# Kernel tuning notes

Hardware: AMD Instinct MI355X
Metric: run time of the kernel (lower is better)

Reference implementation:

```python
import jax, jax.numpy as jnp
import numpy as np

K = 4096
N = 11008
GROUP_SIZE = 128
NUM_GROUPS = K // GROUP_SIZE
BATCH = 4
SEQ = 2048


def setup_inputs() -> dict:
    key = jax.random.key(0)
    kx, kw, ks = jax.random.split(key, 3)
    x = jax.random.normal(kx, (BATCH, SEQ, K), dtype=jnp.float16)
    # packed uint8 bytes, each holding two INT4 values (stored as int32)
    weight_packed = jax.random.randint(kw, (N, K // 2), 0, 256, dtype=jnp.int32)
    # positive group-wise scales ~ abs(randn)*0.1 -> uniform*0.1 is fine statistically
    scales = (jax.random.uniform(ks, (N, NUM_GROUPS), dtype=jnp.float32) * 0.1).astype(jnp.float16)
    return {"x": x, "weight_packed": weight_packed, "scales": scales}


def _dequantize(weight_packed, scales):
    # unpack: low nibble first, then high nibble -> (N, K) values in [0, 15]
    low = weight_packed & 15
    high = (weight_packed >> 4) & 15
    w_int = jnp.stack([low, high], axis=-1).reshape(weight_packed.shape[0], -1)  # (N, K)
    # symmetric dequant with implicit zero-point 8, group-wise scales
    scales_expanded = jnp.repeat(scales, GROUP_SIZE, axis=1)  # (N, K)
    return scales_expanded * (w_int.astype(jnp.float16) - jnp.float16(8.0))


def reference(x, weight_packed, scales):
    # Y = X @ W_dequant.T : (B, S, K) x (N, K) -> (B, S, N)
    w_dequant = _dequantize(weight_packed, scales)  # (N, K) fp16
    out = jnp.einsum('bsk,nk->bsn', x, w_dequant)
    return out.astype(jnp.float16)
```

## Files before the change

### kernel.cpp

```cpp
#include <hip/hip_runtime.h>
#include <stdint.h>


namespace {

typedef unsigned int u32;
typedef unsigned short u16;
typedef __attribute__((ext_vector_type(8))) short bf16x8;
typedef __attribute__((ext_vector_type(4))) float f32x4;
typedef __attribute__((ext_vector_type(4))) u32 u32x4;

constexpr int Mt = 8192;
constexpr int Nt = 11008;
constexpr int Kt = 4096;
constexpr int KP = Kt / 2;
constexpr int NG = 32;
constexpr int BM = 256;
constexpr int BN = 256;
constexpr int BK = 64;
constexpr int THREADS = 512;
constexpr int GRID = (Mt / BM) * (Nt / BN);
constexpr int NKT = Kt / BK;
constexpr int NB_CNT = Nt / BN;

__device__ __forceinline__ u16 f2bf(float f) {
  u32 u = __float_as_uint(f);
  return (u16)((u + 0x7FFFu + ((u >> 16) & 1u)) >> 16);
}
__device__ __forceinline__ u32 pk2bf(float a, float b) {
  return (u32)f2bf(a) | ((u32)f2bf(b) << 16);
}
__device__ __forceinline__ u32 dqpair(u32 b, float s, float c) {
  float f0 = (float)(b & 15u);
  float f1 = (float)((b >> 4) & 15u);
  return pk2bf(fmaf(f0, s, c), fmaf(f1, s, c));
}
__device__ __forceinline__ void async16(const void* g, void* l) {
  __builtin_amdgcn_global_load_lds(
      (const __attribute__((address_space(1))) u32*)g,
      (__attribute__((address_space(3))) u32*)l, 16, 0, 0);
}

__global__ __launch_bounds__(256) void cvt_x(const float* __restrict__ X,
                                             u32* __restrict__ O) {
  const int total = Mt * Kt / 4;
  for (int j = blockIdx.x * 256 + threadIdx.x; j < total;
       j += (int)(gridDim.x * 256)) {
    float4 v = ((const float4*)X)[j];
    ((uint2*)O)[j] = make_uint2(pk2bf(v.x, v.y), pk2bf(v.z, v.w));
  }
}

__global__ __launch_bounds__(256) void cvt_w(const int* __restrict__ W,
                                             const float* __restrict__ S,
                                             u32* __restrict__ O) {
  const int total = Nt * KP / 4;
  for (int j = blockIdx.x * 256 + threadIdx.x; j < total;
       j += (int)(gridDim.x * 256)) {
    int4 v = ((const int4*)W)[j];
    int vv[4] = {v.x, v.y, v.z, v.w};
    const int j0 = j * 4;
    const int row = j0 >> 11;
    const int jj = j0 & 2047;
    const float* sr = S + (size_t)row * NG;
    u32x4 o;
    #pragma unroll
    for (int e = 0; e < 4; ++e) {
      float s = sr[(jj + e) >> 6];
      o[e] = dqpair((u32)vv[e], s, -8.f * s);
    }
    ((u32x4*)O)[j] = o;
  }
}

__global__ __launch_bounds__(THREADS, 2) void gemm8p(
    const u16* __restrict__ Xb, const u16* __restrict__ Wb,
    float* __restrict__ Y) {
  __shared__ __align__(16) unsigned char smem[131072];

  const int tid  = (int)threadIdx.x;
  const int lane = tid & 63;
  const int wid  = tid >> 6;
  const int wm   = wid >> 2;
  const int wn   = wid & 3;

  const int bid = (int)blockIdx.x;
  const int wg  = (bid & 7) * (GRID / 8) + (bid >> 3);
  const int band = wg / 344;
  const int r    = wg - band * 344;
  int mb, nb;
  if (r < 320) {
    const int qn = r >> 5;
    const int w  = r & 31;
    mb = band * 8 + (w >> 2);
    nb = qn * 4 + (w & 3);
  } else {
    const int r2 = r - 320;
    const int q3 = r2 / 3;
    mb = band * 8 + q3;
    nb = 40 + (r2 - q3 * 3);
  }
  const int m0  = mb * BM;
  const int n0  = nb * BN;

  const int srow = tid >> 3;
  const int sswz = (tid & 7) ^ (srow & 7);
  const u16* aRow = Xb + (size_t)(m0 + srow) * Kt + sswz * 8;
  const u16* bRow = Wb + (size_t)(n0 + (srow >> 5) * 64 + (srow & 31)) * Kt + sswz * 8;
  const int ldst = tid * 16;

  const int frow = lane & 15;
  const int fk   = lane >> 4;
  const int s0o  = ((fk ^ (lane & 7)) << 4);
  const int s1o  = (((4 + fk) ^ (lane & 7)) << 4);
  const int aRdC = (wm * 64 + frow) * 128;
  const int bRdC = (wn * 32 + frow) * 128;

  f32x4 acc[8][4];
  #pragma unroll
  for (int i = 0; i < 8; ++i)
    #pragma unroll
    for (int j = 0; j < 4; ++j) acc[i][j] = f32x4{0.f, 0.f, 0.f, 0.f};

  #define GATE(n) asm volatile("s_waitcnt vmcnt(" #n ")" ::: "memory")
  #define BARR()  asm volatile("s_barrier" ::: "memory")

  #define STAGE_A(g, buf, kt)                                                  \
    do {                                                                       \
      unsigned char* d_ = smem + (buf) * 32768 + (g) * 16384 + ldst;           \
      const u16* s_ = aRow + (size_t)((g) * 64) * Kt + (kt) * 64;              \
      async16(s_, d_);                                                         \
      async16(s_ + (size_t)128 * Kt, d_ + 8192);                               \
    } while (0)
  #define STAGE_B(p, buf, kt)                                                  \
    do {                                                                       \
      unsigned char* d_ = smem + 65536 + (buf) * 32768 + (p) * 16384 + ldst;   \
      const u16* s_ = bRow + (size_t)((p) * 32) * Kt + (kt) * 64;              \
      async16(s_, d_);                                                         \
      async16(s_ + (size_t)128 * Kt, d_ + 8192);                               \
    } while (0)

  #define LD_A(dst, g, buf)                                                    \
    do {                                                                       \
      const unsigned char* b_ = smem + (buf) * 32768 + (g) * 16384 + aRdC;     \
      _Pragma("unroll")                                                        \
      for (int q_ = 0; q_ < 4; ++q_) {                                         \
        dst[q_][0] = *(const bf16x8*)(b_ + q_ * 2048 + s0o);                   \
        dst[q_][1] = *(const bf16x8*)(b_ + q_ * 2048 + s1o);                   \
      }                                                                        \
    } while (0)
  #define LD_B(dst, p, buf)                                                    \
    do {                                                                       \
      const unsigned char* b_ =                                                \
          smem + 65536 + (buf) * 32768 + (p) * 16384 + bRdC;                   \
      _Pragma("unroll")                                                        \
      for (int q_ = 0; q_ < 2; ++q_) {                                         \
        dst[q_][0] = *(const bf16x8*)(b_ + q_ * 2048 + s0o);                   \
        dst[q_][1] = *(const bf16x8*)(b_ + q_ * 2048 + s1o);                   \
      }                                                                        \
    } while (0)

  #define MM_G(FG, FNP, A_, B_, GN)                                            \
    do {                                                                       \
      BARR();                                                                  \
      __builtin_amdgcn_s_setprio(1);                                           \
      _Pragma("unroll")                                                        \
      for (int kk_ = 0; kk_ < 2; ++kk_)                                        \
        _Pragma("unroll")                                                      \
        for (int fm_ = 0; fm_ < 4; ++fm_)                                      \
          _Pragma("unroll")                                                    \
          for (int fn_ = 0; fn_ < 2; ++fn_)                                    \
            acc[(FG) * 4 + fm_][(FNP) * 2 + fn_] =                             \
                __builtin_amdgcn_mfma_f32_16x16x32_bf16(                       \
                    A_[fm_][kk_], B_[fn_][kk_],                                \
                    acc[(FG) * 4 + fm_][(FNP) * 2 + fn_], 0, 0, 0);            \
      __builtin_amdgcn_s_setprio(0);                                           \
      if ((GN) == 6) { asm volatile("s_waitcnt vmcnt(6)" ::: "memory"); }      \
      else if ((GN) == 0) { asm volatile("s_waitcnt vmcnt(0)" ::: "memory"); } \
      BARR();                                                                  \
    } while (0)

  #define TILE(BUF, T, GN_LAST)                                                \
    do {                                                                       \
      LD_A(af, 0, BUF);                                                        \
      LD_B(b0, 0, BUF);                                                        \
      STAGE_A(1, BUF ^ 1, (T) + 1);                                            \
      MM_G(0, 0, af, b0, -1);                                                  \
      LD_B(b1, 1, BUF);                                                        \
      STAGE_A(0, BUF, (T) + 2);                                                \
      MM_G(0, 1, af, b1, -1);                                                  \
      LD_A(af, 1, BUF);                                                        \
      STAGE_B(0, BUF, (T) + 2);                                                \
      MM_G(1, 0, af, b0, -1);                                                  \
      STAGE_B(1, BUF, (T) + 2);                                                \
      MM_G(1, 1, af, b1, GN_LAST);                                             \
    } while (0)

  bf16x8 af[4][2], b0[2][2], b1[2][2];

  STAGE_A(0, 0, 0);
  STAGE_B(0, 0, 0);
  STAGE_B(1, 0, 0);
  STAGE_A(1, 0, 0);
  STAGE_A(0, 1, 1);
  STAGE_B(0, 1, 1);
  STAGE_B(1, 1, 1);
  GATE(6);
  BARR();

  #pragma unroll 1
  for (int t0 = 0; t0 < NKT - 2; t0 += 2) {
    TILE(0, t0, 6);
    TILE(1, t0 + 1, 6);
  }

  {
    LD_A(af, 0, 0);
    LD_B(b0, 0, 0);
    STAGE_A(1, 1, 63);
    MM_G(0, 0, af, b0, -1);
    LD_B(b1, 1, 0);
    MM_G(0, 1, af, b1, -1);
    LD_A(af, 1, 0);
    MM_G(1, 0, af, b0, -1);
    MM_G(1, 1, af, b1, 0);
  }
  {
    LD_A(af, 0, 1);
    LD_B(b0, 0, 1);
    MM_G(0, 0, af, b0, -1);
    LD_B(b1, 1, 1);
    MM_G(0, 1, af, b1, -1);
    LD_A(af, 1, 1);
    MM_G(1, 0, af, b0, -1);
    MM_G(1, 1, af, b1, -1);
  }

  #undef GATE
  #undef BARR
  #undef STAGE_A
  #undef STAGE_B
  #undef LD_A
  #undef LD_B
  #undef MM_G
  #undef TILE

  #pragma unroll
  for (int fm = 0; fm < 8; ++fm) {
    #pragma unroll
    for (int r2 = 0; r2 < 4; ++r2) {
      const size_t mrow = (size_t)(m0 + wm * 128 + fm * 16 + fk * 4 + r2) * Nt;
      #pragma unroll
      for (int fn = 0; fn < 4; ++fn) {
        Y[mrow + (size_t)(n0 + wn * 64 + fn * 16 + frow)] = acc[fm][fn][r2];
      }
    }
  }
}

__global__ __launch_bounds__(512) void gemm_fused(
    const float* __restrict__ Xf, const int* __restrict__ W,
    const float* __restrict__ S, float* __restrict__ Y) {
  constexpr int FBN = 128;
  constexpr int FNB = Nt / FBN;
  constexpr int FBK = 64;
  constexpr int FNKT = Kt / FBK;
  __shared__ __align__(16) unsigned char Alds[BM * FBK * 2];
  __shared__ __align__(16) unsigned char Blds[FBN * FBK * 2];

  const int tid = (int)threadIdx.x;
  const int lane = tid & 63;
  const int wid = tid >> 6;
  const int wm = wid >> 1;
  const int wn = wid & 1;

  const int bid = (int)blockIdx.x;
  const int fgrid = (Mt / BM) * FNB;
  const int wg = (bid & 7) * (fgrid / 8) + (bid >> 3);
  const int mb = wg / FNB;
  const int nb = wg - mb * FNB;
  const int m0 = mb * BM;
  const int n0 = nb * FBN;

  const int frow = lane & 15;
  const int fk = lane >> 4;
  const int fswz = (lane & 7) << 4;
  const unsigned char* aRd = Alds + (wm * 64 + frow) * 128;
  const unsigned char* bRd = Blds + (wn * 64 + frow) * 128;

  f32x4 acc[4][4];
  #pragma unroll
  for (int i = 0; i < 4; ++i)
    #pragma unroll
    for (int j = 0; j < 4; ++j) acc[i][j] = f32x4{0.f, 0.f, 0.f, 0.f};

  const int arow = tid >> 3, acol = tid & 7;
  const float* fA = Xf + (size_t)(m0 + arow) * Kt + acol * 8;
  unsigned char* fAD = Alds + arow * 128 + ((acol ^ (arow & 7)) << 4);
  const int nloc = tid >> 3, c4 = tid & 7;
  const int* fB0 = W + (size_t)(n0 + nloc) * KP + c4 * 4;
  const int* fB1 = fB0 + (size_t)64 * KP;
  const float* sp0 = S + (size_t)(n0 + nloc) * NG;
  const float* sp1 = sp0 + (size_t)64 * NG;
  unsigned char* fBD0 = Blds + nloc * 128 + ((c4 ^ (nloc & 7)) << 4);
  unsigned char* fBD1 = fBD0 + 64 * 128;

  #pragma unroll 1
  for (int kt = 0; kt < FNKT; ++kt) {
    const int k0 = kt * FBK;
    #pragma unroll
    for (int p = 0; p < 4; ++p) {
      float4 x0 = *(const float4*)(fA + (size_t)p * 64 * Kt + k0);
      float4 x1 = *(const float4*)(fA + (size_t)p * 64 * Kt + k0 + 4);
      u32x4 q;
      q[0] = pk2bf(x0.x, x0.y); q[1] = pk2bf(x0.z, x0.w);
      q[2] = pk2bf(x1.x, x1.y); q[3] = pk2bf(x1.z, x1.w);
      *(u32x4*)(fAD + p * 64 * 128) = q;
    }
    const int g = k0 >> 7;
    const float s0 = sp0[g], s1 = sp1[g];
    const float c0 = -8.f * s0, c1 = -8.f * s1;
    const int4 w0 = *(const int4*)(fB0 + (k0 >> 1));
    const int4 w1 = *(const int4*)(fB1 + (k0 >> 1));
    u32x4 q0, q1;
    q0[0] = dqpair((u32)w0.x, s0, c0); q0[1] = dqpair((u32)w0.y, s0, c0);
    q0[2] = dqpair((u32)w0.z, s0, c0); q0[3] = dqpair((u32)w0.w, s0, c0);
    q1[0] = dqpair((u32)w1.x, s1, c1); q1[1] = dqpair((u32)w1.y, s1, c1);
    q1[2] = dqpair((u32)w1.z, s1, c1); q1[3] = dqpair((u32)w1.w, s1, c1);
    *(u32x4*)fBD0 = q0;
    *(u32x4*)fBD1 = q1;

    __syncthreads();

    #pragma unroll
    for (int kk = 0; kk < 2; ++kk) {
      const int koff = (kk * 64 + fk * 16) ^ fswz;
      bf16x8 af[4], bfr[4];
      #pragma unroll
      for (int fm = 0; fm < 4; ++fm)
        af[fm] = *(const bf16x8*)(aRd + fm * 16 * 128 + koff);
      #pragma unroll
      for (int fn = 0; fn < 4; ++fn)
        bfr[fn] = *(const bf16x8*)(bRd + fn * 16 * 128 + koff);
      #pragma unroll
      for (int fm = 0; fm < 4; ++fm)
        #pragma unroll
        for (int fn = 0; fn < 4; ++fn)
          acc[fm][fn] = __builtin_amdgcn_mfma_f32_16x16x32_bf16(
              af[fm], bfr[fn], acc[fm][fn], 0, 0, 0);
    }
    __syncthreads();
  }

  #pragma unroll
  for (int fm = 0; fm < 4; ++fm) {
    #pragma unroll
    for (int r = 0; r < 4; ++r) {
      const size_t mrow = (size_t)(m0 + wm * 64 + fm * 16 + fk * 4 + r) * Nt;
      #pragma unroll
      for (int fn = 0; fn < 4; ++fn)
        Y[mrow + (size_t)(n0 + wn * 64 + fn * 16 + frow)] = acc[fm][fn][r];
    }
  }
}

}

extern "C" void kernel_launch(void* const* d_in, const int* in_sizes, int n_in,
                              void* d_out, int out_size, void* d_ws, size_t ws_size,
                              hipStream_t stream) {
  (void)in_sizes; (void)n_in; (void)out_size;
  const float* X = (const float*)d_in[0];
  const int* W   = (const int*)d_in[1];
  const float* S = (const float*)d_in[2];
  float* Y       = (float*)d_out;

  const size_t xbytes = (size_t)Mt * Kt * 2;
  const size_t wbytes = (size_t)Nt * Kt * 2;

  if (ws_size >= xbytes + wbytes) {
    u16* Xb = (u16*)d_ws;
    u16* Wb = (u16*)((char*)d_ws + xbytes);
    cvt_x<<<dim3(2048), dim3(256), 0, stream>>>(X, (u32*)Xb);
    cvt_w<<<dim3(2048), dim3(256), 0, stream>>>(W, S, (u32*)Wb);
    gemm8p<<<dim3(GRID), dim3(THREADS), 0, stream>>>(Xb, Wb, Y);
  } else {
    gemm_fused<<<dim3((Mt / BM) * (Nt / 128)), dim3(512), 0, stream>>>(X, W, S, Y);
  }
}
```

Measured before the change: 676.4 us.

## Double-buffer register fragments to prefetch next tile's LDS reads across phases

```diff
diff --git a/kernel.cpp b/kernel.cpp
--- a/kernel.cpp
+++ b/kernel.cpp
@@ -73,7 +73,7 @@
   }
 }
 
-__global__ __launch_bounds__(THREADS, 2) void gemm8p(
+__global__ __launch_bounds__(THREADS, 2) void gemmrl(
     const u16* __restrict__ Xb, const u16* __restrict__ Wb,
     float* __restrict__ Y) {
   __shared__ __align__(16) unsigned char smem[131072];
@@ -160,9 +160,8 @@
       }                                                                        \
     } while (0)
 
-  #define MM_G(FG, FNP, A_, B_, GN)                                            \
-    do {                                                                       \
-      BARR();                                                                  \
+  #define MMQ(FG, FNP, A_, B_)                                                 \
+    do {                                                                       \
       __builtin_amdgcn_s_setprio(1);                                           \
       _Pragma("unroll")                                                        \
       for (int kk_ = 0; kk_ < 2; ++kk_)                                        \
@@ -175,28 +174,45 @@
                     A_[fm_][kk_], B_[fn_][kk_],                                \
                     acc[(FG) * 4 + fm_][(FNP) * 2 + fn_], 0, 0, 0);            \
       __builtin_amdgcn_s_setprio(0);                                           \
-      if ((GN) == 6) { asm volatile("s_waitcnt vmcnt(6)" ::: "memory"); }      \
-      else if ((GN) == 0) { asm volatile("s_waitcnt vmcnt(0)" ::: "memory"); } \
-      BARR();                                                                  \
-    } while (0)
-
-  #define TILE(BUF, T, GN_LAST)                                                \
-    do {                                                                       \
-      LD_A(af, 0, BUF);                                                        \
-      LD_B(b0, 0, BUF);                                                        \
-      STAGE_A(1, BUF ^ 1, (T) + 1);                                            \
-      MM_G(0, 0, af, b0, -1);                                                  \
-      LD_B(b1, 1, BUF);                                                        \
-      STAGE_A(0, BUF, (T) + 2);                                                \
-      MM_G(0, 1, af, b1, -1);                                                  \
-      LD_A(af, 1, BUF);                                                        \
-      STAGE_B(0, BUF, (T) + 2);                                                \
-      MM_G(1, 0, af, b0, -1);                                                  \
-      STAGE_B(1, BUF, (T) + 2);                                                \
-      MM_G(1, 1, af, b1, GN_LAST);                                             \
-    } while (0)
-
-  bf16x8 af[4][2], b0[2][2], b1[2][2];
+    } while (0)
+
+  #define OPTGATE(G)                                                           \
+    do {                                                                       \
+      if ((G) == 6) { asm volatile("s_waitcnt vmcnt(6)" ::: "memory"); }       \
+      else if ((G) == 0) { asm volatile("s_waitcnt vmcnt(0)" ::: "memory"); }  \
+    } while (0)
+
+  #define TILE(BUF, T, S1, S2, S3, S4, G1, G2)                                 \
+    do {                                                                       \
+                    \
+      LD_B(bB, 1, BUF);                                                        \
+      if (S1) STAGE_A(1, (BUF) ^ 1, (T) + 1);                                  \
+      BARR();                                                                  \
+      MMQ(0, 0, afA, bA);                                                      \
+      BARR();                                                                  \
+            \
+      LD_A(afB, 1, BUF);                                                       \
+      if (S2) STAGE_A(0, BUF, (T) + 2);                                        \
+      BARR();                                                                  \
+      MMQ(0, 1, afA, bB);                                                      \
+      OPTGATE(G1);                                                             \
+      BARR();                                                                  \
+                \
+      LD_A(afA, 0, (BUF) ^ 1);                                                 \
+      if (S3) STAGE_B(0, BUF, (T) + 2);                                        \
+      BARR();                                                                  \
+      MMQ(1, 0, afB, bA);                                                      \
+      BARR();                                                                  \
+            \
+      LD_B(bA, 0, (BUF) ^ 1);                                                  \
+      if (S4) STAGE_B(1, BUF, (T) + 2);                                        \
+      BARR();                                                                  \
+      MMQ(1, 1, afB, bB);                                                      \
+      OPTGATE(G2);                                                             \
+      BARR();                                                                  \
+    } while (0)
+
+  bf16x8 afA[4][2], afB[4][2], bA[2][2], bB[2][2];
 
   STAGE_A(0, 0, 0);
   STAGE_B(0, 0, 0);
@@ -207,33 +223,22 @@
   STAGE_B(1, 1, 1);
   GATE(6);
   BARR();
+  LD_A(afA, 0, 0);
+  LD_B(bA, 0, 0);
 
   #pragma unroll 1
   for (int t0 = 0; t0 < NKT - 2; t0 += 2) {
-    TILE(0, t0, 6);
-    TILE(1, t0 + 1, 6);
-  }
-
+    TILE(0, t0,     1, 1, 1, 1, 6, 6);
+    TILE(1, t0 + 1, 1, 1, 1, 1, 6, 6);
+  }
+  TILE(0, 62, 1, 0, 0, 0, 6, 0);
   {
-    LD_A(af, 0, 0);
-    LD_B(b0, 0, 0);
-    STAGE_A(1, 1, 63);
-    MM_G(0, 0, af, b0, -1);
-    LD_B(b1, 1, 0);
-    MM_G(0, 1, af, b1, -1);
-    LD_A(af, 1, 0);
-    MM_G(1, 0, af, b0, -1);
-    MM_G(1, 1, af, b1, 0);
-  }
-  {
-    LD_A(af, 0, 1);
-    LD_B(b0, 0, 1);
-    MM_G(0, 0, af, b0, -1);
-    LD_B(b1, 1, 1);
-    MM_G(0, 1, af, b1, -1);
-    LD_A(af, 1, 1);
-    MM_G(1, 0, af, b0, -1);
-    MM_G(1, 1, af, b1, -1);
+    LD_B(bB, 1, 1);
+    LD_A(afB, 1, 1);
+    MMQ(0, 0, afA, bA);
+    MMQ(0, 1, afA, bB);
+    MMQ(1, 0, afB, bA);
+    MMQ(1, 1, afB, bB);
   }
 
   #undef GATE
@@ -242,7 +247,8 @@
   #undef STAGE_B
   #undef LD_A
   #undef LD_B
-  #undef MM_G
+  #undef MMQ
+  #undef OPTGATE
   #undef TILE
 
   #pragma unroll
@@ -383,7 +389,7 @@
     u16* Wb = (u16*)((char*)d_ws + xbytes);
     cvt_x<<<dim3(2048), dim3(256), 0, stream>>>(X, (u32*)Xb);
     cvt_w<<<dim3(2048), dim3(256), 0, stream>>>(W, S, (u32*)Wb);
-    gemm8p<<<dim3(GRID), dim3(THREADS), 0, stream>>>(Xb, Wb, Y);
+    gemmrl<<<dim3(GRID), dim3(THREADS), 0, stream>>>(Xb, Wb, Y);
   } else {
     gemm_fused<<<dim3((Mt / BM) * (Nt / 128)), dim3(512), 0, stream>>>(X, W, S, Y);
   }
```

Result: slower. 913.1 us (+35.0%).
